# Kernel tuning notes

Measured on AMD Instinct MI355X. Metric: run time of the kernel, lower is better.

The kernel has to match this reference:

```python
import jax, jax.numpy as jnp
import numpy as np

B, T, C, H, MEM = 2, 2048, 1024, 16, 256
HD = C // H


def setup_inputs() -> dict:
    key = jax.random.key(0)
    ks = jax.random.split(key, 6)
    return {
        "x": jax.random.normal(ks[0], (B, T, C), dtype=jnp.float32),
        "ext_mem": jax.random.normal(ks[1], (B, MEM, C), dtype=jnp.float32),
        "W_attn": jax.random.normal(ks[2], (C, 3 * C), dtype=jnp.float32) * 0.02,
        "b_attn": jax.random.normal(ks[3], (3 * C,), dtype=jnp.float32) * 0.02,
        "W_proj": jax.random.normal(ks[4], (C, C), dtype=jnp.float32) * 0.02,
        "b_proj": jax.random.normal(ks[5], (C,), dtype=jnp.float32) * 0.02,
    }


def reference(x, ext_mem, W_attn, b_attn, W_proj, b_proj):
    Bx, Tx, Cx = x.shape
    qkv = x @ W_attn + b_attn                      # [B,T,3C]
    q, k, v = jnp.split(qkv, 3, axis=-1)
    # [B,H,T,HD]
    q = q.reshape(Bx, Tx, H, HD).transpose(0, 2, 1, 3)
    k = k.reshape(Bx, Tx, H, HD).transpose(0, 2, 1, 3)
    v = v.reshape(Bx, Tx, H, HD).transpose(0, 2, 1, 3)
    mem = ext_mem.reshape(Bx, -1, H, HD).transpose(0, 2, 1, 3)  # [B,H,MEM,HD]
    k = jnp.concatenate([mem, k], axis=2)          # [B,H,MEM+T,HD]
    v = jnp.concatenate([mem, v], axis=2)
    mem_len = k.shape[2] - Tx
    scale = 1.0 / jnp.sqrt(jnp.float32(HD))
    att = jnp.einsum("bhtd,bhsd->bhts", q, k) * scale  # [B,H,T,MEM+T]
    # memory prefix fully attended; causal over the T query positions
    rows = jnp.arange(Tx)[:, None]
    cols = jnp.arange(mem_len + Tx)[None, :]
    allowed = (cols < mem_len) | ((cols - mem_len) <= rows)  # [T,MEM+T]
    att = jnp.where(allowed[None, None], att, jnp.float32(-jnp.inf))
    att = jax.nn.softmax(att, axis=-1)
    y = jnp.einsum("bhts,bhsd->bhtd", att, v)      # [B,H,T,HD]
    y = y.transpose(0, 2, 1, 3).reshape(Bx, Tx, Cx)
    return y @ W_proj + b_proj
```

## Files before the change

kernel.cpp:

```cpp
#include <hip/hip_runtime.h>

#define B_    2
#define T_    2048
#define C_    1024
#define H_    16
#define HD_   64
#define MEM_  256
#define S_    2304
#define NKT_  36

typedef __attribute__((ext_vector_type(8))) short short8;
typedef __attribute__((ext_vector_type(4))) short short4v;
typedef __attribute__((ext_vector_type(4))) float f32x4;

__device__ __forceinline__ unsigned short f2bf(float x) {
    return (unsigned short)((__float_as_uint(x) + 0x8000u) >> 16);
}

__device__ __forceinline__ unsigned int pk2bf(float lo, float hi) {
    unsigned int a = __float_as_uint(lo) + 0x8000u;
    unsigned int b = __float_as_uint(hi) + 0x8000u;
    return __builtin_amdgcn_perm(b, a, 0x07060302);
}

typedef const __attribute__((address_space(1))) unsigned int* gp_t;
typedef __attribute__((address_space(3))) unsigned int* lp_t;

__device__ __forceinline__ void gll16(const unsigned short* g, unsigned short* l) {
    __builtin_amdgcn_global_load_lds((gp_t)g, (lp_t)l, 16, 0, 0);
}

#define C1_ 0.18033688011112042f

__global__ __launch_bounds__(256) void prep_all(
    const float* __restrict__ x, const float* __restrict__ Wa,
    const float* __restrict__ Wp, const float* __restrict__ ext,
    unsigned short* __restrict__ x_tl, unsigned short* __restrict__ WtA,
    unsigned short* __restrict__ WtP, unsigned short* __restrict__ k_ws,
    unsigned short* __restrict__ v_tl)
{
    __shared__ float L[64][65];
    const int bid = blockIdx.x, tid = threadIdx.x;
    if (bid < 4096) {
        int i = bid * 256 + tid;
        int c = (i & 255) * 4;
        int m = i >> 8;
        float4 v = ((const float4*)x)[i];
        ushort4 o;
        o.x = f2bf(v.x); o.y = f2bf(v.y); o.z = f2bf(v.z); o.w = f2bf(v.w);
        int mt = m >> 7, r = m & 127, kc = c >> 5, cc = c & 31;
        int p = (cc >> 3) ^ ((r >> 1) & 3);
        *(ushort4*)&x_tl[(((size_t)mt * 32 + kc) << 12) + (r << 5) + p * 8 + (cc & 7)] = o;
    } else if (bid < 5120) {
        const float* in; unsigned short* out; int Cc, r0, c0;
        if (bid < 4864) {
            int r = bid - 4096; in = Wa; out = WtA; Cc = 3 * C_;
            c0 = (r % 48) * 64; r0 = (r / 48) * 64;
        } else {
            int r = bid - 4864; in = Wp; out = WtP; Cc = C_;
            c0 = (r & 15) * 64; r0 = (r >> 4) * 64;
        }
        const int jj = tid >> 4;
        const int i4 = (tid & 15) * 4;
#pragma unroll
        for (int t = 0; t < 4; ++t) {
            int j = jj + t * 16;
            float4 v = *(const float4*)(in + (size_t)(r0 + j) * Cc + c0 + i4);
            L[i4 + 0][j] = v.x; L[i4 + 1][j] = v.y;
            L[i4 + 2][j] = v.z; L[i4 + 3][j] = v.w;
        }
        __syncthreads();
#pragma unroll
        for (int t = 0; t < 4; ++t) {
            int n = c0 + jj + t * 16;
            int k = r0 + i4;
            ushort4 o;
            o.x = f2bf(L[jj + t * 16][i4 + 0]); o.y = f2bf(L[jj + t * 16][i4 + 1]);
            o.z = f2bf(L[jj + t * 16][i4 + 2]); o.w = f2bf(L[jj + t * 16][i4 + 3]);
            int nt = n >> 7, r = n & 127, kc = k >> 5, cc = k & 31;
            int p = (cc >> 3) ^ ((r >> 1) & 3);
            *(ushort4*)&out[(((size_t)nt * 32 + kc) << 12) + (r << 5) + p * 8 + (cc & 7)] = o;
        }
    } else {
        int idx = (bid - 5120) * 256 + tid;
        float val = ext[idx];
        int c = idx & (C_ - 1), m = (idx >> 10) & (MEM_ - 1), b = idx >> 18;
        int h = c >> 6, d = c & 63;
        int bh = b * H_ + h;
        unsigned short bv = f2bf(val);
        k_ws[(size_t)bh * S_ * 64 + (size_t)m * 64 + (((d >> 3) ^ (m & 7)) << 3) + (d & 7)] = bv;
        int ts = m >> 6, key = m & 63;
        v_tl[(((size_t)bh * NKT_ + ts) * 64 + d) * 64 + (((key >> 3) ^ (d & 7)) << 3) + (key & 7)] = bv;
    }
}

__global__ __launch_bounds__(256) void qkv_gemm(
    const unsigned short* __restrict__ A,
    const unsigned short* __restrict__ Bt,
    const float* __restrict__ bias,
    unsigned short* __restrict__ q_ws,
    unsigned short* __restrict__ k_ws,
    unsigned short* __restrict__ v_tl)
{
    __shared__ __align__(16) unsigned short As[2][4096];
    __shared__ __align__(16) unsigned short Bs[2][4096];
    const int tid = threadIdx.x, lane = tid & 63, wave = tid >> 6;
    const int wr = wave >> 1, wc = wave & 1;
    const size_t abase = (size_t)blockIdx.y * 32 * 4096;
    const size_t bbase = (size_t)blockIdx.x * 32 * 4096;

    f32x4 acc[4][4];
#pragma unroll
    for (int i = 0; i < 4; ++i)
#pragma unroll
        for (int j = 0; j < 4; ++j) acc[i][j] = (f32x4){0.f, 0.f, 0.f, 0.f};

    auto stage = [&](int kc, int buf) {
        const unsigned short* ga = A + abase + (size_t)kc * 4096;
        const unsigned short* gb = Bt + bbase + (size_t)kc * 4096;
#pragma unroll
        for (int s = 0; s < 2; ++s) {
            int seg = wave + s * 4;
            gll16(ga + seg * 512 + lane * 8, &As[buf][seg * 512]);
            gll16(gb + seg * 512 + lane * 8, &Bs[buf][seg * 512]);
        }
    };

    stage(0, 0);
    __syncthreads();
    for (int kc = 0; kc < 32; ++kc) {
        if (kc + 1 < 32) stage(kc + 1, (kc + 1) & 1);
        const unsigned short* as = As[kc & 1];
        const unsigned short* bs = Bs[kc & 1];
        short8 af[4], bf4[4];
#pragma unroll
        for (int i = 0; i < 4; ++i) {
            int row = wr * 64 + i * 16 + (lane & 15);
            int ph = (lane >> 4) ^ ((row >> 1) & 3);
            af[i] = *(const short8*)&as[row * 32 + ph * 8];
        }
#pragma unroll
        for (int j = 0; j < 4; ++j) {
            int row = wc * 64 + j * 16 + (lane & 15);
            int ph = (lane >> 4) ^ ((row >> 1) & 3);
            bf4[j] = *(const short8*)&bs[row * 32 + ph * 8];
        }
#pragma unroll
        for (int i = 0; i < 4; ++i)
#pragma unroll
            for (int j = 0; j < 4; ++j)
                acc[i][j] = __builtin_amdgcn_mfma_f32_16x16x32_bf16(
                    af[i], bf4[j], acc[i][j], 0, 0, 0);
        __syncthreads();
    }

#pragma unroll
    for (int j = 0; j < 4; ++j) {
        int n = blockIdx.x * 128 + wc * 64 + j * 16 + (lane & 15);
        float bs = bias[n];
        int sel = n >> 10, h = (n >> 6) & 15, d = n & 63;
#pragma unroll
        for (int i = 0; i < 4; ++i) {
            int m = blockIdx.y * 128 + wr * 64 + i * 16 + (lane >> 4) * 4;
            int b = m >> 11, t0 = m & (T_ - 1);
            int bh = b * H_ + h;
            if (sel == 0) {
                size_t base = ((size_t)bh * T_ + t0) * 64 + d;
#pragma unroll
                for (int r = 0; r < 4; ++r)
                    q_ws[base + (size_t)r * 64] = f2bf((acc[i][j][r] + bs) * C1_);
            } else if (sel == 1) {
#pragma unroll
                for (int r = 0; r < 4; ++r) {
                    int s = MEM_ + t0 + r;
                    k_ws[(size_t)bh * S_ * 64 + (size_t)s * 64
                         + (((d >> 3) ^ (s & 7)) << 3) + (d & 7)] =
                        f2bf(acc[i][j][r] + bs);
                }
            } else {
                int s0 = MEM_ + t0, ts = s0 >> 6, key = s0 & 63;
                ushort4 pv;
                pv.x = f2bf(acc[i][j][0] + bs);
                pv.y = f2bf(acc[i][j][1] + bs);
                pv.z = f2bf(acc[i][j][2] + bs);
                pv.w = f2bf(acc[i][j][3] + bs);
                *(ushort4*)&v_tl[(((size_t)bh * NKT_ + ts) * 64 + d) * 64
                                 + (((key >> 3) ^ (d & 7)) << 3) + (key & 7)] = pv;
            }
        }
    }
}

__global__ __launch_bounds__(256) void proj_gemm(
    const unsigned short* __restrict__ A,
    const unsigned short* __restrict__ Bt,
    const float* __restrict__ bias,
    float* __restrict__ out)
{
    __shared__ __align__(16) unsigned short As[2][2048];
    __shared__ __align__(16) unsigned short Bs[2][4096];
    const int tid = threadIdx.x, lane = tid & 63, wave = tid >> 6;
    const int m64 = blockIdx.y;
    const size_t abase = ((size_t)(m64 >> 1) * 32) * 4096 + (size_t)(m64 & 1) * 2048;
    const size_t bbase = (size_t)blockIdx.x * 32 * 4096;

    f32x4 acc[4][2];
#pragma unroll
    for (int i = 0; i < 4; ++i)
#pragma unroll
        for (int j = 0; j < 2; ++j) acc[i][j] = (f32x4){0.f, 0.f, 0.f, 0.f};

    auto stage = [&](int kc, int buf) {
        const unsigned short* ga = A + abase + (size_t)kc * 4096;
        const unsigned short* gb = Bt + bbase + (size_t)kc * 4096;
        gll16(ga + wave * 512 + lane * 8, &As[buf][wave * 512]);
        gll16(gb + wave * 512 + lane * 8, &Bs[buf][wave * 512]);
        gll16(gb + (wave + 4) * 512 + lane * 8, &Bs[buf][(wave + 4) * 512]);
    };

    stage(0, 0);
    __syncthreads();
    for (int kc = 0; kc < 32; ++kc) {
        if (kc + 1 < 32) stage(kc + 1, (kc + 1) & 1);
        const unsigned short* as = As[kc & 1];
        const unsigned short* bs = Bs[kc & 1];
        short8 af[4], bf2[2];
#pragma unroll
        for (int i = 0; i < 4; ++i) {
            int row = i * 16 + (lane & 15);
            int ph = (lane >> 4) ^ ((row >> 1) & 3);
            af[i] = *(const short8*)&as[row * 32 + ph * 8];
        }
#pragma unroll
        for (int j = 0; j < 2; ++j) {
            int row = wave * 32 + j * 16 + (lane & 15);
            int ph = (lane >> 4) ^ ((row >> 1) & 3);
            bf2[j] = *(const short8*)&bs[row * 32 + ph * 8];
        }
#pragma unroll
        for (int i = 0; i < 4; ++i)
#pragma unroll
            for (int j = 0; j < 2; ++j)
                acc[i][j] = __builtin_amdgcn_mfma_f32_16x16x32_bf16(
                    af[i], bf2[j], acc[i][j], 0, 0, 0);
        __syncthreads();
    }

#pragma unroll
    for (int j = 0; j < 2; ++j) {
        int n = blockIdx.x * 128 + wave * 32 + j * 16 + (lane & 15);
        float bs = bias[n];
#pragma unroll
        for (int i = 0; i < 4; ++i) {
            int m = m64 * 64 + i * 16 + (lane >> 4) * 4;
#pragma unroll
            for (int r = 0; r < 4; ++r)
                out[(size_t)(m + r) * C_ + n] = acc[i][j][r] + bs;
        }
    }
}

__global__ __launch_bounds__(512, 4) void flash_mfma(
    const unsigned short* __restrict__ qg,
    const unsigned short* __restrict__ kg,
    const unsigned short* __restrict__ vg,
    unsigned short* __restrict__ yt)
{
    __shared__ __align__(16) unsigned short Ks[4][4096];
    __shared__ __align__(16) unsigned short Vs[4][4096];

    const int tid = threadIdx.x, lane = tid & 63, w = tid >> 6;
    const int grp = w >> 2, wq = w & 3;
    const int quad = lane >> 4;
    const int a = blockIdx.x;
    const int h = blockIdx.y, b = blockIdx.z;
    const int p0 = 5 + a;
    const int nl = 36 - a;
    const int n2 = nl - p0;
    const int qt = grp ? (31 - a) : a;
    const int bh = b * H_ + h;
    const size_t kgb = (size_t)bh * S_ * 64;
    const size_t vgb = (size_t)bh * NKT_ * 4096;

    short8 qfP[2], qf2[2];
    {
        const unsigned short* p = qg + ((size_t)bh * T_ + qt * 64 + wq * 16
                                        + (lane & 15)) * 64 + quad * 8;
        qfP[0] = *(const short8*)p; qfP[1] = *(const short8*)(p + 32);
        const unsigned short* q2 = qg + ((size_t)bh * T_ + (31 - a) * 64 + wq * 16
                                         + (lane & 15)) * 64 + quad * 8;
        qf2[0] = *(const short8*)q2; qf2[1] = *(const short8*)(q2 + 32);
    }

    f32x4 o[4], o2[4];
#pragma unroll
    for (int j = 0; j < 4; ++j) {
        o[j] = (f32x4){0.f, 0.f, 0.f, 0.f};
        o2[j] = (f32x4){0.f, 0.f, 0.f, 0.f};
    }
    float l = 0.f, l2 = 0.f;

    const unsigned short* kB0 = &Ks[0][(lane & 15) * 64 + ((quad ^ (lane & 7)) * 8)];
    const unsigned short* kB1 = &Ks[0][(lane & 15) * 64 + (((quad + 4) ^ (lane & 7)) * 8)];
    const unsigned short* vPs[4];
#pragma unroll
    for (int kb = 0; kb < 4; ++kb)
        vPs[kb] = &Vs[0][(lane & 15) * 64
                         + (((kb * 2 + (lane >> 5)) ^ (lane & 7)) * 8)
                         + (quad & 1) * 4];

    auto stageTo = [&](int kt) {
        const int bf = kt & 3;
        const unsigned short* gk = kg + kgb + (size_t)kt * 4096;
        const unsigned short* gv = vg + vgb + (size_t)kt * 4096;
        gll16(gk + w * 512 + lane * 8, &Ks[bf][w * 512]);
        gll16(gv + w * 512 + lane * 8, &Vs[bf][w * 512]);
    };

    const int tqP = qt * 64 + wq * 16 + (lane & 15);
    const int tq2 = (31 - a) * 64 + wq * 16 + (lane & 15);

    auto computeTile = [&](int kt, const short8 (&qf)[2], f32x4 (&oo)[4],
                           float& ll, bool diag, int tq) {
        const int B = (kt & 3) << 12;
        const int s0 = kt * 64;
        short8 kA[4][2];
#pragma unroll
        for (int kb = 0; kb < 4; ++kb) {
            kA[kb][0] = *(const short8*)&kB0[B + kb * 1024];
            kA[kb][1] = *(const short8*)&kB1[B + kb * 1024];
        }
        short4v vF[4][4];
#pragma unroll
        for (int kb = 0; kb < 4; ++kb)
#pragma unroll
            for (int dblk = 0; dblk < 4; ++dblk)
                vF[kb][dblk] = *(const short4v*)&vPs[kb][B + dblk * 1024];

#pragma unroll
        for (int kb = 0; kb < 4; ++kb) {
            f32x4 z = (f32x4){0.f, 0.f, 0.f, 0.f};
            z = __builtin_amdgcn_mfma_f32_16x16x32_bf16(kA[kb][0], qf[0], z, 0, 0, 0);
            z = __builtin_amdgcn_mfma_f32_16x16x32_bf16(kA[kb][1], qf[1], z, 0, 0, 0);
            float p[4];
#pragma unroll
            for (int r = 0; r < 4; ++r) {
                float e = exp2f(z[r]);
                if (diag) {
                    int key = s0 + kb * 16 + quad * 4 + r;
                    if (key - MEM_ > tq) e = 0.f;
                }
                ll += e;
                p[r] = e;
            }
            short4v pf;
            *(unsigned int*)&pf       = pk2bf(p[0], p[1]);
            *((unsigned int*)&pf + 1) = pk2bf(p[2], p[3]);
#pragma unroll
            for (int dblk = 0; dblk < 4; ++dblk)
                oo[dblk] = __builtin_amdgcn_mfma_f32_16x16x16bf16_1k(
                    pf, vF[kb][dblk], oo[dblk], 0, 0, 0);
        }
    };

    stageTo(0); stageTo(1); stageTo(2);
    int cursor = 3;

    for (int s = 0; s < p0; ++s) {
        __syncthreads();
        if (cursor < nl && cursor <= s + 3) { stageTo(cursor); ++cursor; }
        computeTile(s, qfP, o, l, (grp == 0) && (s == p0 - 1), tqP);
    }

    const int nsteps2 = (n2 + 1) >> 1;
    for (int s2 = 0; s2 < nsteps2; ++s2) {
        __syncthreads();
        while (cursor < nl && cursor <= p0 + 2 * s2 + 3) { stageTo(cursor); ++cursor; }
        int t = p0 + 2 * s2 + grp;
        if (t < nl) {
            bool dg = (t == nl - 1);
            if (grp == 0) computeTile(t, qf2, o2, l2, dg, tq2);
            else          computeTile(t, qfP, o, l, dg, tqP);
        }
    }

    __syncthreads();
    float* sm = (float*)&Ks[0][0];
    if (grp == 0) {
        int idx = (wq * 64 + lane) * 17;
#pragma unroll
        for (int dblk = 0; dblk < 4; ++dblk)
#pragma unroll
            for (int r = 0; r < 4; ++r) sm[idx + dblk * 4 + r] = o2[dblk][r];
        sm[idx + 16] = l2;
    }
    __syncthreads();
    if (grp == 1) {
        int idx = (wq * 64 + lane) * 17;
#pragma unroll
        for (int dblk = 0; dblk < 4; ++dblk)
#pragma unroll
            for (int r = 0; r < 4; ++r) o[dblk][r] += sm[idx + dblk * 4 + r];
        l += sm[idx + 16];
    }

    l += __shfl_xor(l, 16);
    l += __shfl_xor(l, 32);
    float linv[4];
#pragma unroll
    for (int r = 0; r < 4; ++r)
        linv[r] = 1.f / __shfl(l, quad * 4 + r);
#pragma unroll
    for (int dblk = 0; dblk < 4; ++dblk) {
        int c = h * 64 + dblk * 16 + (lane & 15);
        int kc = c >> 5, cc = c & 31;
#pragma unroll
        for (int r = 0; r < 4; ++r) {
            int t = qt * 64 + wq * 16 + quad * 4 + r;
            int m = b * T_ + t;
            int mt = m >> 7, rr = m & 127;
            int p = (cc >> 3) ^ ((rr >> 1) & 3);
            yt[(((size_t)mt * 32 + kc) << 12) + (rr << 5) + p * 8 + (cc & 7)] =
                f2bf(o[dblk][r] * linv[r]);
        }
    }
}

extern "C" void kernel_launch(void* const* d_in, const int* in_sizes, int n_in,
                              void* d_out, int out_size, void* d_ws, size_t ws_size,
                              hipStream_t stream) {
    (void)in_sizes; (void)n_in; (void)out_size; (void)ws_size;
    const float* x      = (const float*)d_in[0];
    const float* ext    = (const float*)d_in[1];
    const float* W_attn = (const float*)d_in[2];
    const float* b_attn = (const float*)d_in[3];
    const float* W_proj = (const float*)d_in[4];
    const float* b_proj = (const float*)d_in[5];
    float* out = (float*)d_out;

    unsigned short* x_tl  = (unsigned short*)d_ws;
    unsigned short* WtA   = x_tl + 4194304;
    unsigned short* WtP   = WtA + 3145728;
    unsigned short* q_ws  = WtP + 1048576;
    unsigned short* k_ws  = q_ws + 4194304;
    unsigned short* v_tl  = k_ws + 4718592;
    unsigned short* y_tl  = v_tl + 4718592;

    dim3 blk(256);
    prep_all<<<7168, blk, 0, stream>>>(x, W_attn, W_proj, ext,
                                       x_tl, WtA, WtP, k_ws, v_tl);
    qkv_gemm<<<dim3(24, 32), blk, 0, stream>>>(
        x_tl, WtA, b_attn, q_ws, k_ws, v_tl);
    flash_mfma<<<dim3(16, H_, B_), dim3(512), 0, stream>>>(q_ws, k_ws, v_tl, y_tl);
    proj_gemm<<<dim3(8, 64), blk, 0, stream>>>(y_tl, WtP, b_proj, out);
}
```

Baseline: 196.7 us.

## Halve flash block to 4 waves, each computing two 16-row query subtiles

The attention kernel now runs 256 threads per block instead of 512. Each wave handles 32 query rows as two 16-row subtiles, so every K/V fragment loaded from shared memory feeds twice as many MFMAs. This cuts LDS read traffic per unit of work and doubles the register-held accumulators and Q fragments per wave. In exchange, register pressure rises, each wave issues twice the staging loads, and fewer waves are available to hide latency.

Result: slower. 205.5 us (+4.5%).

```diff
diff --git a/kernel.cpp b/kernel.cpp
--- a/kernel.cpp
+++ b/kernel.cpp
@@ -260,7 +260,7 @@
     }
 }
 
-__global__ __launch_bounds__(512, 4) void flash_mfma(
+__global__ __launch_bounds__(256, 2) void flash_mfma(
     const unsigned short* __restrict__ qg,
     const unsigned short* __restrict__ kg,
     const unsigned short* __restrict__ vg,
@@ -270,35 +270,40 @@
     __shared__ __align__(16) unsigned short Vs[4][4096];
 
     const int tid = threadIdx.x, lane = tid & 63, w = tid >> 6;
-    const int grp = w >> 2, wq = w & 3;
+    const int g  = w >> 1;
+    const int wq = w & 1;
     const int quad = lane >> 4;
     const int a = blockIdx.x;
     const int h = blockIdx.y, b = blockIdx.z;
     const int p0 = 5 + a;
     const int nl = 36 - a;
     const int n2 = nl - p0;
-    const int qt = grp ? (31 - a) : a;
+    const int qt = g ? (31 - a) : a;
     const int bh = b * H_ + h;
     const size_t kgb = (size_t)bh * S_ * 64;
     const size_t vgb = (size_t)bh * NKT_ * 4096;
 
-    short8 qfP[2], qf2[2];
+    short8 qfP[2][2], qf2[2][2];
     {
-        const unsigned short* p = qg + ((size_t)bh * T_ + qt * 64 + wq * 16
-                                        + (lane & 15)) * 64 + quad * 8;
-        qfP[0] = *(const short8*)p; qfP[1] = *(const short8*)(p + 32);
-        const unsigned short* q2 = qg + ((size_t)bh * T_ + (31 - a) * 64 + wq * 16
+        const unsigned short* q1 = qg + ((size_t)bh * T_ + qt * 64 + wq * 32
                                          + (lane & 15)) * 64 + quad * 8;
-        qf2[0] = *(const short8*)q2; qf2[1] = *(const short8*)(q2 + 32);
-    }
-
-    f32x4 o[4], o2[4];
-#pragma unroll
-    for (int j = 0; j < 4; ++j) {
-        o[j] = (f32x4){0.f, 0.f, 0.f, 0.f};
-        o2[j] = (f32x4){0.f, 0.f, 0.f, 0.f};
-    }
-    float l = 0.f, l2 = 0.f;
+        qfP[0][0] = *(const short8*)q1;          qfP[0][1] = *(const short8*)(q1 + 32);
+        qfP[1][0] = *(const short8*)(q1 + 1024); qfP[1][1] = *(const short8*)(q1 + 1056);
+        const unsigned short* q2 = qg + ((size_t)bh * T_ + (31 - a) * 64 + wq * 32
+                                         + (lane & 15)) * 64 + quad * 8;
+        qf2[0][0] = *(const short8*)q2;          qf2[0][1] = *(const short8*)(q2 + 32);
+        qf2[1][0] = *(const short8*)(q2 + 1024); qf2[1][1] = *(const short8*)(q2 + 1056);
+    }
+
+    f32x4 o[2][4], o2[2][4];
+#pragma unroll
+    for (int s = 0; s < 2; ++s)
+#pragma unroll
+        for (int j = 0; j < 4; ++j) {
+            o[s][j] = (f32x4){0.f, 0.f, 0.f, 0.f};
+            o2[s][j] = (f32x4){0.f, 0.f, 0.f, 0.f};
+        }
+    float l[2] = {0.f, 0.f}, l2[2] = {0.f, 0.f};
 
     const unsigned short* kB0 = &Ks[0][(lane & 15) * 64 + ((quad ^ (lane & 7)) * 8)];
     const unsigned short* kB1 = &Ks[0][(lane & 15) * 64 + (((quad + 4) ^ (lane & 7)) * 8)];
@@ -313,15 +318,20 @@
         const int bf = kt & 3;
         const unsigned short* gk = kg + kgb + (size_t)kt * 4096;
         const unsigned short* gv = vg + vgb + (size_t)kt * 4096;
-        gll16(gk + w * 512 + lane * 8, &Ks[bf][w * 512]);
-        gll16(gv + w * 512 + lane * 8, &Vs[bf][w * 512]);
+        const int sg = w * 2;
+        gll16(gk + sg * 512 + lane * 8,       &Ks[bf][sg * 512]);
+        gll16(gk + (sg + 1) * 512 + lane * 8, &Ks[bf][(sg + 1) * 512]);
+        gll16(gv + sg * 512 + lane * 8,       &Vs[bf][sg * 512]);
+        gll16(gv + (sg + 1) * 512 + lane * 8, &Vs[bf][(sg + 1) * 512]);
     };
 
-    const int tqP = qt * 64 + wq * 16 + (lane & 15);
-    const int tq2 = (31 - a) * 64 + wq * 16 + (lane & 15);
-
-    auto computeTile = [&](int kt, const short8 (&qf)[2], f32x4 (&oo)[4],
-                           float& ll, bool diag, int tq) {
+    const int tqP0 = qt * 64 + wq * 32 + (lane & 15);
+    const int tqP1 = tqP0 + 16;
+    const int tq20 = (31 - a) * 64 + wq * 32 + (lane & 15);
+    const int tq21 = tq20 + 16;
+
+    auto computeTile = [&](int kt, const short8 (&qf)[2][2], f32x4 (&oo)[2][4],
+                           float (&ll)[2], bool diag, int tqa, int tqb) {
         const int B = (kt & 3) << 12;
         const int s0 = kt * 64;
         short8 kA[4][2];
@@ -339,27 +349,37 @@
 
 #pragma unroll
         for (int kb = 0; kb < 4; ++kb) {
-            f32x4 z = (f32x4){0.f, 0.f, 0.f, 0.f};
-            z = __builtin_amdgcn_mfma_f32_16x16x32_bf16(kA[kb][0], qf[0], z, 0, 0, 0);
-            z = __builtin_amdgcn_mfma_f32_16x16x32_bf16(kA[kb][1], qf[1], z, 0, 0, 0);
-            float p[4];
+            f32x4 z0 = (f32x4){0.f, 0.f, 0.f, 0.f};
+            f32x4 z1 = (f32x4){0.f, 0.f, 0.f, 0.f};
+            z0 = __builtin_amdgcn_mfma_f32_16x16x32_bf16(kA[kb][0], qf[0][0], z0, 0, 0, 0);
+            z0 = __builtin_amdgcn_mfma_f32_16x16x32_bf16(kA[kb][1], qf[0][1], z0, 0, 0, 0);
+            z1 = __builtin_amdgcn_mfma_f32_16x16x32_bf16(kA[kb][0], qf[1][0], z1, 0, 0, 0);
+            z1 = __builtin_amdgcn_mfma_f32_16x16x32_bf16(kA[kb][1], qf[1][1], z1, 0, 0, 0);
+            float p0v[4], p1v[4];
 #pragma unroll
             for (int r = 0; r < 4; ++r) {
-                float e = exp2f(z[r]);
+                float e0 = exp2f(z0[r]);
+                float e1 = exp2f(z1[r]);
                 if (diag) {
                     int key = s0 + kb * 16 + quad * 4 + r;
-                    if (key - MEM_ > tq) e = 0.f;
+                    if (key - MEM_ > tqa) e0 = 0.f;
+                    if (key - MEM_ > tqb) e1 = 0.f;
                 }
-                ll += e;
-                p[r] = e;
+                ll[0] += e0; p0v[r] = e0;
+                ll[1] += e1; p1v[r] = e1;
             }
-            short4v pf;
-            *(unsigned int*)&pf       = pk2bf(p[0], p[1]);
-            *((unsigned int*)&pf + 1) = pk2bf(p[2], p[3]);
-#pragma unroll
-            for (int dblk = 0; dblk < 4; ++dblk)
-                oo[dblk] = __builtin_amdgcn_mfma_f32_16x16x16bf16_1k(
-                    pf, vF[kb][dblk], oo[dblk], 0, 0, 0);
+            short4v pf0, pf1;
+            *(unsigned int*)&pf0       = pk2bf(p0v[0], p0v[1]);
+            *((unsigned int*)&pf0 + 1) = pk2bf(p0v[2], p0v[3]);
+            *(unsigned int*)&pf1       = pk2bf(p1v[0], p1v[1]);
+            *((unsigned int*)&pf1 + 1) = pk2bf(p1v[2], p1v[3]);
+#pragma unroll
+            for (int dblk = 0; dblk < 4; ++dblk) {
+                oo[0][dblk] = __builtin_amdgcn_mfma_f32_16x16x16bf16_1k(
+                    pf0, vF[kb][dblk], oo[0][dblk], 0, 0, 0);
+                oo[1][dblk] = __builtin_amdgcn_mfma_f32_16x16x16bf16_1k(
+                    pf1, vF[kb][dblk], oo[1][dblk], 0, 0, 0);
+            }
         }
     };
 
@@ -369,59 +389,71 @@
     for (int s = 0; s < p0; ++s) {
         __syncthreads();
         if (cursor < nl && cursor <= s + 3) { stageTo(cursor); ++cursor; }
-        computeTile(s, qfP, o, l, (grp == 0) && (s == p0 - 1), tqP);
+        computeTile(s, qfP, o, l, (g == 0) && (s == p0 - 1), tqP0, tqP1);
     }
 
     const int nsteps2 = (n2 + 1) >> 1;
     for (int s2 = 0; s2 < nsteps2; ++s2) {
         __syncthreads();
         while (cursor < nl && cursor <= p0 + 2 * s2 + 3) { stageTo(cursor); ++cursor; }
-        int t = p0 + 2 * s2 + grp;
+        int t = p0 + 2 * s2 + g;
         if (t < nl) {
             bool dg = (t == nl - 1);
-            if (grp == 0) computeTile(t, qf2, o2, l2, dg, tq2);
-            else          computeTile(t, qfP, o, l, dg, tqP);
+            if (g == 0) computeTile(t, qf2, o2, l2, dg, tq20, tq21);
+            else        computeTile(t, qfP, o, l, dg, tqP0, tqP1);
         }
     }
 
     __syncthreads();
     float* sm = (float*)&Ks[0][0];
-    if (grp == 0) {
-        int idx = (wq * 64 + lane) * 17;
-#pragma unroll
-        for (int dblk = 0; dblk < 4; ++dblk)
-#pragma unroll
-            for (int r = 0; r < 4; ++r) sm[idx + dblk * 4 + r] = o2[dblk][r];
-        sm[idx + 16] = l2;
+    if (g == 0) {
+        int idx = (wq * 64 + lane) * 34;
+#pragma unroll
+        for (int sb = 0; sb < 2; ++sb)
+#pragma unroll
+            for (int dblk = 0; dblk < 4; ++dblk)
+#pragma unroll
+                for (int r = 0; r < 4; ++r)
+                    sm[idx + sb * 16 + dblk * 4 + r] = o2[sb][dblk][r];
+        sm[idx + 32] = l2[0];
+        sm[idx + 33] = l2[1];
     }
     __syncthreads();
-    if (grp == 1) {
-        int idx = (wq * 64 + lane) * 17;
-#pragma unroll
-        for (int dblk = 0; dblk < 4; ++dblk)
-#pragma unroll
-            for (int r = 0; r < 4; ++r) o[dblk][r] += sm[idx + dblk * 4 + r];
-        l += sm[idx + 16];
-    }
-
-    l += __shfl_xor(l, 16);
-    l += __shfl_xor(l, 32);
-    float linv[4];
-#pragma unroll
-    for (int r = 0; r < 4; ++r)
-        linv[r] = 1.f / __shfl(l, quad * 4 + r);
-#pragma unroll
-    for (int dblk = 0; dblk < 4; ++dblk) {
-        int c = h * 64 + dblk * 16 + (lane & 15);
-        int kc = c >> 5, cc = c & 31;
-#pragma unroll
-        for (int r = 0; r < 4; ++r) {
-            int t = qt * 64 + wq * 16 + quad * 4 + r;
-            int m = b * T_ + t;
-            int mt = m >> 7, rr = m & 127;
-            int p = (cc >> 3) ^ ((rr >> 1) & 3);
-            yt[(((size_t)mt * 32 + kc) << 12) + (rr << 5) + p * 8 + (cc & 7)] =
-                f2bf(o[dblk][r] * linv[r]);
+    if (g == 1) {
+        int idx = (wq * 64 + lane) * 34;
+#pragma unroll
+        for (int sb = 0; sb < 2; ++sb)
+#pragma unroll
+            for (int dblk = 0; dblk < 4; ++dblk)
+#pragma unroll
+                for (int r = 0; r < 4; ++r)
+                    o[sb][dblk][r] += sm[idx + sb * 16 + dblk * 4 + r];
+        l[0] += sm[idx + 32];
+        l[1] += sm[idx + 33];
+    }
+
+#pragma unroll
+    for (int sb = 0; sb < 2; ++sb) {
+        float ls = l[sb];
+        ls += __shfl_xor(ls, 16);
+        ls += __shfl_xor(ls, 32);
+        float linv[4];
+#pragma unroll
+        for (int r = 0; r < 4; ++r)
+            linv[r] = 1.f / __shfl(ls, quad * 4 + r);
+#pragma unroll
+        for (int dblk = 0; dblk < 4; ++dblk) {
+            int c = h * 64 + dblk * 16 + (lane & 15);
+            int kc = c >> 5, cc = c & 31;
+#pragma unroll
+            for (int r = 0; r < 4; ++r) {
+                int t = qt * 64 + wq * 32 + sb * 16 + quad * 4 + r;
+                int m = b * T_ + t;
+                int mt = m >> 7, rr = m & 127;
+                int pp = (cc >> 3) ^ ((rr >> 1) & 3);
+                yt[(((size_t)mt * 32 + kc) << 12) + (rr << 5) + pp * 8 + (cc & 7)] =
+                    f2bf(o[sb][dblk][r] * linv[r]);
+            }
         }
     }
 }
@@ -451,6 +483,6 @@
                                        x_tl, WtA, WtP, k_ws, v_tl);
     qkv_gemm<<<dim3(24, 32), blk, 0, stream>>>(
         x_tl, WtA, b_attn, q_ws, k_ws, v_tl);
-    flash_mfma<<<dim3(16, H_, B_), dim3(512), 0, stream>>>(q_ws, k_ws, v_tl, y_tl);
+    flash_mfma<<<dim3(16, H_, B_), blk, 0, stream>>>(q_ws, k_ws, v_tl, y_tl);
     proj_gemm<<<dim3(8, 64), blk, 0, stream>>>(y_tl, WtP, b_proj, out);
 }
```

## Compute softmax row sums via MFMA with ones and remap blocks across XCDs

Applied to the files above, without the earlier changes.

The softmax denominator is now accumulated with an extra bf16 MFMA against a ones vector, replacing the per-element scalar adds and the final cross-lane shuffles. The sums are formed from the bf16-rounded probabilities, so they match the numerator exactly. Block indices are remapped so that consecutive blocks sharing a head land on the same XCD, aiming for better L2 reuse of K/V. Staging pointers are also advanced incrementally instead of being recomputed for each tile. The trade-off is one extra MFMA per key block, against fewer VALU adds and shuffles.

Measured after the change: 193.5 us. No clear change (-1.6%).

```diff
diff --git a/kernel.cpp b/kernel.cpp
--- a/kernel.cpp
+++ b/kernel.cpp
@@ -272,8 +272,12 @@
     const int tid = threadIdx.x, lane = tid & 63, w = tid >> 6;
     const int grp = w >> 2, wq = w & 3;
     const int quad = lane >> 4;
-    const int a = blockIdx.x;
-    const int h = blockIdx.y, b = blockIdx.z;
+    const int flat = blockIdx.x + 16 * (blockIdx.y + 16 * blockIdx.z);
+    const int xcd = flat & 7;
+    const int kk = flat >> 3;
+    const int a = kk & 15;
+    const int g8 = (kk >> 4) * 8 + xcd;
+    const int h = g8 & 15, b = g8 >> 4;
     const int p0 = 5 + a;
     const int nl = 36 - a;
     const int n2 = nl - p0;
@@ -298,7 +302,15 @@
         o[j] = (f32x4){0.f, 0.f, 0.f, 0.f};
         o2[j] = (f32x4){0.f, 0.f, 0.f, 0.f};
     }
-    float l = 0.f, l2 = 0.f;
+    f32x4 lv  = (f32x4){0.f, 0.f, 0.f, 0.f};
+    f32x4 lv2 = (f32x4){0.f, 0.f, 0.f, 0.f};
+
+    short4v ones;
+    {
+        unsigned int oo1 = 0x3F803F80u;
+        *(unsigned int*)&ones = oo1;
+        *((unsigned int*)&ones + 1) = oo1;
+    }
 
     const unsigned short* kB0 = &Ks[0][(lane & 15) * 64 + ((quad ^ (lane & 7)) * 8)];
     const unsigned short* kB1 = &Ks[0][(lane & 15) * 64 + (((quad + 4) ^ (lane & 7)) * 8)];
@@ -309,19 +321,21 @@
                          + (((kb * 2 + (lane >> 5)) ^ (lane & 7)) * 8)
                          + (quad & 1) * 4];
 
-    auto stageTo = [&](int kt) {
+    const unsigned short* gkC = kg + kgb + (size_t)w * 512 + (size_t)lane * 8;
+    const unsigned short* gvC = vg + vgb + (size_t)w * 512 + (size_t)lane * 8;
+
+    auto stageCur = [&](int kt) {
         const int bf = kt & 3;
-        const unsigned short* gk = kg + kgb + (size_t)kt * 4096;
-        const unsigned short* gv = vg + vgb + (size_t)kt * 4096;
-        gll16(gk + w * 512 + lane * 8, &Ks[bf][w * 512]);
-        gll16(gv + w * 512 + lane * 8, &Vs[bf][w * 512]);
+        gll16(gkC, &Ks[bf][w * 512]);
+        gll16(gvC, &Vs[bf][w * 512]);
+        gkC += 4096; gvC += 4096;
     };
 
     const int tqP = qt * 64 + wq * 16 + (lane & 15);
     const int tq2 = (31 - a) * 64 + wq * 16 + (lane & 15);
 
     auto computeTile = [&](int kt, const short8 (&qf)[2], f32x4 (&oo)[4],
-                           float& ll, bool diag, int tq) {
+                           f32x4& lacc, bool diag, int tq) {
         const int B = (kt & 3) << 12;
         const int s0 = kt * 64;
         short8 kA[4][2];
@@ -350,12 +364,13 @@
                     int key = s0 + kb * 16 + quad * 4 + r;
                     if (key - MEM_ > tq) e = 0.f;
                 }
-                ll += e;
                 p[r] = e;
             }
             short4v pf;
             *(unsigned int*)&pf       = pk2bf(p[0], p[1]);
             *((unsigned int*)&pf + 1) = pk2bf(p[2], p[3]);
+            lacc = __builtin_amdgcn_mfma_f32_16x16x16bf16_1k(
+                pf, ones, lacc, 0, 0, 0);
 #pragma unroll
             for (int dblk = 0; dblk < 4; ++dblk)
                 oo[dblk] = __builtin_amdgcn_mfma_f32_16x16x16bf16_1k(
@@ -363,53 +378,53 @@
         }
     };
 
-    stageTo(0); stageTo(1); stageTo(2);
+    stageCur(0); stageCur(1); stageCur(2);
     int cursor = 3;
 
     for (int s = 0; s < p0; ++s) {
         __syncthreads();
-        if (cursor < nl && cursor <= s + 3) { stageTo(cursor); ++cursor; }
-        computeTile(s, qfP, o, l, (grp == 0) && (s == p0 - 1), tqP);
+        if (cursor < nl && cursor <= s + 3) { stageCur(cursor); ++cursor; }
+        computeTile(s, qfP, o, lv, (grp == 0) && (s == p0 - 1), tqP);
     }
 
     const int nsteps2 = (n2 + 1) >> 1;
     for (int s2 = 0; s2 < nsteps2; ++s2) {
         __syncthreads();
-        while (cursor < nl && cursor <= p0 + 2 * s2 + 3) { stageTo(cursor); ++cursor; }
+        while (cursor < nl && cursor <= p0 + 2 * s2 + 3) { stageCur(cursor); ++cursor; }
         int t = p0 + 2 * s2 + grp;
         if (t < nl) {
             bool dg = (t == nl - 1);
-            if (grp == 0) computeTile(t, qf2, o2, l2, dg, tq2);
-            else          computeTile(t, qfP, o, l, dg, tqP);
+            if (grp == 0) computeTile(t, qf2, o2, lv2, dg, tq2);
+            else          computeTile(t, qfP, o, lv, dg, tqP);
         }
     }
 
     __syncthreads();
     float* sm = (float*)&Ks[0][0];
     if (grp == 0) {
-        int idx = (wq * 64 + lane) * 17;
+        int idx = (wq * 64 + lane) * 20;
 #pragma unroll
         for (int dblk = 0; dblk < 4; ++dblk)
 #pragma unroll
             for (int r = 0; r < 4; ++r) sm[idx + dblk * 4 + r] = o2[dblk][r];
-        sm[idx + 16] = l2;
+#pragma unroll
+        for (int r = 0; r < 4; ++r) sm[idx + 16 + r] = lv2[r];
     }
     __syncthreads();
     if (grp == 1) {
-        int idx = (wq * 64 + lane) * 17;
+        int idx = (wq * 64 + lane) * 20;
 #pragma unroll
         for (int dblk = 0; dblk < 4; ++dblk)
 #pragma unroll
             for (int r = 0; r < 4; ++r) o[dblk][r] += sm[idx + dblk * 4 + r];
-        l += sm[idx + 16];
-    }
-
-    l += __shfl_xor(l, 16);
-    l += __shfl_xor(l, 32);
+#pragma unroll
+        for (int r = 0; r < 4; ++r) lv[r] += sm[idx + 16 + r];
+    }
+
     float linv[4];
 #pragma unroll
     for (int r = 0; r < 4; ++r)
-        linv[r] = 1.f / __shfl(l, quad * 4 + r);
+        linv[r] = 1.f / lv[r];
 #pragma unroll
     for (int dblk = 0; dblk < 4; ++dblk) {
         int c = h * 64 + dblk * 16 + (lane & 15);
```
